# Kernel optimization log

Measured on AMD Instinct MI355X. Metric: run time of the kernel, lower is better.

## Reference

```python
import jax, jax.numpy as jnp
import numpy as np

# 'normal' eta table from the original module (19 fault modes x 4 params)
_NORMAL_ETA = np.array([
    [-0.044411, -0.95086, -0.0169, -142.23],
    [0.83907, -1.0, 0.0, 2.0978e-17],
    [-0.60647, -1.0, 0.0, 1.0867e-08],
    [-0.99992, -1.0, 0.0, -4.5596e-18],
    [0.83907, -1.0, 0.0, -1.8533e-17],
    [31.485, 0.0028551, -0.09998, 6.3016],
    [-1.0, -1.0, 0.0, 4.407e-16],
    [183.07, -183.94, -83.575, 0.042966],
    [-0.60647, -1.0, 0.0, 1.0867e-08],
    [0.12159, -0.73578, -0.079441, 3.109],
    [0.83907, -1.0, 0.0, 2.0978e-17],
    [-0.99992, -1.0, 0.0, -4.5596e-18],
    [0.76517, -0.0080291, 0.63714, 1.2184],
    [0.83907, -1.0, 0.0, 2.0978e-17],
    [0.83907, -1.0, 0.0, -1.8533e-17],
    [-1.0, -1.0, 0.0, 4.407e-16],
    [1.0, -1.0, 0.0, 4.4982e-16],
    [-0.045913, -0.72633, 0.073493, 10.507],
    [-0.99992, -1.0, 0.0, -4.5596e-18],
], dtype=np.float32)

M, N, B, L = 8, 64, 512, 128  # Mask rows, N_train, batch, mask entries per row


def setup_inputs() -> dict:
    key = jax.random.key(0)
    k_z, k_m = jax.random.split(key)
    z = jax.random.normal(k_z, (M, N, B, L), dtype=jnp.float32)
    eta_fault = jnp.asarray(_NORMAL_ETA)  # [19, 4]
    Mask = jax.random.randint(k_m, (M, L), 0, 19, dtype=jnp.int64)
    return {"z": z, "eta_fault": eta_fault, "Mask": Mask}


def reference(z, eta_fault, Mask):
    # Gather per-(mask-row, entry) eta params: [M, L, 4]
    eta = eta_fault[Mask]
    # Broadcast against z [M, N, B, L]: eta components become [M, 1, 1, L]
    e0 = eta[:, None, None, :, 0]
    e1 = eta[:, None, None, :, 1]
    e2 = eta[:, None, None, :, 2]
    e3 = eta[:, None, None, :, 3]
    return -(e0 + e1 * jnp.tanh((z - e2) * e3))
```

## Files before the change

kernel.cpp:

```cpp
#include <hip/hip_runtime.h>


#define M_DIM 8
#define L_DIM 128
#define NB 32768
#define PER_M 4194304
#define BLOCKS_PER_M 256
#define THREADS 256
#define PER_BLOCK 16384
#define ITERS 16

__device__ __forceinline__ float fast_tanh(float x) {
    float t = __builtin_amdgcn_exp2f(x * 2.8853900817779268f);
    float r = __builtin_amdgcn_rcpf(1.0f + t);
    return __builtin_fmaf(-2.0f, r, 1.0f);
}

__global__ __launch_bounds__(THREADS) void invrt_kernel(
    const float* __restrict__ z,
    const float* __restrict__ eta_fault,
    const int*  __restrict__ mask,
    float* __restrict__ out)
{
    const int tid   = threadIdx.x;
    const int bid   = blockIdx.x;
    const int m     = bid >> 8;
    const int chunk = bid & 255;

    const int l0 = (tid & 31) * 4;

    float a0[4], a1[4], a2[4], a3[4];
#pragma unroll
    for (int j = 0; j < 4; ++j) {
        const int row = mask[m * L_DIM + l0 + j];
        const float4 e = *reinterpret_cast<const float4*>(eta_fault + row * 4);
        a0[j] = -e.x;
        a1[j] = -e.y;
        a2[j] = e.z;
        a3[j] = e.w;
    }

    const long long base = (long long)m * PER_M + (long long)chunk * PER_BLOCK + tid * 4;
    const float* zp = z + base;
    float*       op = out + base;

#pragma unroll 4
    for (int it = 0; it < ITERS; ++it) {
        const float4 zv = *reinterpret_cast<const float4*>(zp + it * (THREADS * 4));
        float4 ov;
        ov.x = __builtin_fmaf(a1[0], fast_tanh((zv.x - a2[0]) * a3[0]), a0[0]);
        ov.y = __builtin_fmaf(a1[1], fast_tanh((zv.y - a2[1]) * a3[1]), a0[1]);
        ov.z = __builtin_fmaf(a1[2], fast_tanh((zv.z - a2[2]) * a3[2]), a0[2]);
        ov.w = __builtin_fmaf(a1[3], fast_tanh((zv.w - a2[3]) * a3[3]), a0[3]);
        *reinterpret_cast<float4*>(op + it * (THREADS * 4)) = ov;
    }
}

extern "C" void kernel_launch(void* const* d_in, const int* in_sizes, int n_in,
                              void* d_out, int out_size, void* d_ws, size_t ws_size,
                              hipStream_t stream) {
    const float* z   = (const float*)d_in[0];
    const float* eta = (const float*)d_in[1];
    const int*   msk = (const int*)d_in[2];
    float*       out = (float*)d_out;

    dim3 grid(M_DIM * BLOCKS_PER_M);
    dim3 block(THREADS);
    invrt_kernel<<<grid, block, 0, stream>>>(z, eta, msk, out);
}
```

Measured before the change: 238.6 us.

## Issue all loads up front, use nontemporal stores, double block count

Each block now handles half as many elements, so the grid has twice as many blocks. Each thread issues all eight float4 loads before computing, which keeps more memory requests in flight. Outputs are written with nontemporal stores so they do not pollute the cache. The cost is more registers per thread and more blocks, each repeating the small eta gather.

```diff
diff --git a/kernel.cpp b/kernel.cpp
--- a/kernel.cpp
+++ b/kernel.cpp
@@ -3,12 +3,14 @@
 
 #define M_DIM 8
 #define L_DIM 128
-#define NB 32768
 #define PER_M 4194304
-#define BLOCKS_PER_M 256
+#define BLOCKS_PER_M 512
 #define THREADS 256
-#define PER_BLOCK 16384
-#define ITERS 16
+#define PER_BLOCK 8192
+#define DEPTH 8
+#define STRIDE (THREADS * 4)
+
+typedef float f32x4 __attribute__((ext_vector_type(4)));
 
 __device__ __forceinline__ float fast_tanh(float x) {
     float t = __builtin_amdgcn_exp2f(x * 2.8853900817779268f);
@@ -16,7 +18,7 @@
     return __builtin_fmaf(-2.0f, r, 1.0f);
 }
 
-__global__ __launch_bounds__(THREADS) void invrt_kernel(
+__global__ __launch_bounds__(THREADS, 1) void invrt_kernel(
     const float* __restrict__ z,
     const float* __restrict__ eta_fault,
     const int*  __restrict__ mask,
@@ -24,8 +26,8 @@
 {
     const int tid   = threadIdx.x;
     const int bid   = blockIdx.x;
-    const int m     = bid >> 8;
-    const int chunk = bid & 255;
+    const int m     = bid >> 9;
+    const int chunk = bid & 511;
 
     const int l0 = (tid & 31) * 4;
 
@@ -33,7 +35,7 @@
 #pragma unroll
     for (int j = 0; j < 4; ++j) {
         const int row = mask[m * L_DIM + l0 + j];
-        const float4 e = *reinterpret_cast<const float4*>(eta_fault + row * 4);
+        const f32x4 e = *reinterpret_cast<const f32x4*>(eta_fault + row * 4);
         a0[j] = -e.x;
         a1[j] = -e.y;
         a2[j] = e.z;
@@ -44,15 +46,19 @@
     const float* zp = z + base;
     float*       op = out + base;
 
-#pragma unroll 4
-    for (int it = 0; it < ITERS; ++it) {
-        const float4 zv = *reinterpret_cast<const float4*>(zp + it * (THREADS * 4));
-        float4 ov;
-        ov.x = __builtin_fmaf(a1[0], fast_tanh((zv.x - a2[0]) * a3[0]), a0[0]);
-        ov.y = __builtin_fmaf(a1[1], fast_tanh((zv.y - a2[1]) * a3[1]), a0[1]);
-        ov.z = __builtin_fmaf(a1[2], fast_tanh((zv.z - a2[2]) * a3[2]), a0[2]);
-        ov.w = __builtin_fmaf(a1[3], fast_tanh((zv.w - a2[3]) * a3[3]), a0[3]);
-        *reinterpret_cast<float4*>(op + it * (THREADS * 4)) = ov;
+    f32x4 v[DEPTH];
+#pragma unroll
+    for (int j = 0; j < DEPTH; ++j)
+        v[j] = *reinterpret_cast<const f32x4*>(zp + j * STRIDE);
+
+#pragma unroll
+    for (int j = 0; j < DEPTH; ++j) {
+        f32x4 o;
+        o.x = __builtin_fmaf(a1[0], fast_tanh((v[j].x - a2[0]) * a3[0]), a0[0]);
+        o.y = __builtin_fmaf(a1[1], fast_tanh((v[j].y - a2[1]) * a3[1]), a0[1]);
+        o.z = __builtin_fmaf(a1[2], fast_tanh((v[j].z - a2[2]) * a3[2]), a0[2]);
+        o.w = __builtin_fmaf(a1[3], fast_tanh((v[j].w - a2[3]) * a3[3]), a0[3]);
+        __builtin_nontemporal_store(o, reinterpret_cast<f32x4*>(op + j * STRIDE));
     }
 }
 
```

After: 232.8 us. 1.02x faster.
